# Kernel tuning notes

Measured on AMD Instinct MI355X. Metric: run time of the kernel, lower is better.

## Reference

```python
import jax, jax.numpy as jnp
import numpy as np
import math

WINDOW = 257
W = (WINDOW - 1) // 2      # 128
Q_CH = WINDOW + 1          # 258 (query chunk size / stride)
K_CH = WINDOW * 2          # 514 (key window size)


def compl_mod(m, n):
    return int(n * math.ceil(m / n) - m)


def setup_inputs() -> dict:
    key = jax.random.key(0)
    k1, k2, k3 = jax.random.split(key, 3)
    b, s, nh, h = 2, 4096, 16, 64
    q = jax.random.normal(k1, (b, s, nh, h), jnp.float32)
    k = jax.random.normal(k2, (b, s, nh, h), jnp.float32)
    v = jax.random.normal(k3, (b, s, nh, h), jnp.float32)
    return {"q": q, "k": k, "v": v}


def reference(q, k, v):
    b, s, nh, h = q.shape
    q = q * h ** (-0.5)
    q_pad = compl_mod(s, Q_CH)
    k_pad = compl_mod(s + 2 * W - K_CH, Q_CH)
    c = (s + q_pad) // Q_CH  # number of chunks

    # pad along sequence dim (q right-padded; k/v haloed by w on both sides)
    qp = jnp.pad(q, ((0, 0), (0, q_pad), (0, 0), (0, 0)))
    kp = jnp.pad(k, ((0, 0), (W, W + k_pad), (0, 0), (0, 0)))
    vp = jnp.pad(v, ((0, 0), (W, W + k_pad), (0, 0), (0, 0)))

    # unfold: q non-overlapping chunks, k/v overlapping windows (size K_CH, stride Q_CH)
    qw = qp.reshape(b, c, Q_CH, nh, h)                              # [b,c,q,nh,h]
    idx = (jnp.arange(c) * Q_CH)[:, None] + jnp.arange(K_CH)[None]  # [c,K_CH]
    kw = kp[:, idx]                                                 # [b,c,k,nh,h]
    vw = vp[:, idx]

    A = jnp.einsum('bcqnh,bcknh->bncqk', qw, kw)  # [b,nh,c,Q_CH,K_CH]

    # banded mask: valid iff i <= j <= i + 2w (True = masked)
    i = jnp.arange(Q_CH)[:, None]
    j = jnp.arange(K_CH)[None, :]
    base = ~((j >= i) & (j <= i + 2 * W))
    mask_left = base.at[:, :W].set(True)                    # first chunk: no left halo
    mask_right = base.at[:, K_CH - (W + k_pad):].set(True)  # last chunk: no right halo/pad
    if c > 1:
        mask = jnp.concatenate(
            [mask_left[None], jnp.broadcast_to(base, (c - 2, Q_CH, K_CH)), mask_right[None]], axis=0)
    else:
        mask = (mask_left | mask_right)[None]

    mask_value = -jnp.finfo(A.dtype).max
    A = jnp.where(mask[None, None], mask_value, A)
    A = jax.nn.softmax(A, axis=-1)  # dropout omitted (eval mode)

    z = jnp.einsum('bncqk,bcknh->bncqh', A, vw)       # [b,nh,c,Q_CH,h]
    z = z.reshape(b, nh, c * Q_CH, h)[:, :, :s]       # trim q padding
    return jnp.transpose(z, (0, 2, 1, 3))             # [b,s,nh,h]
```

## Files before the change

### kernel.cpp

```cpp
#include <hip/hip_runtime.h>

typedef _Float16 h16;
typedef __attribute__((ext_vector_type(2))) _Float16 f16x2;
typedef __attribute__((ext_vector_type(4))) _Float16 f16x4;
typedef __attribute__((ext_vector_type(2))) __fp16   fp16x2n;
typedef __attribute__((ext_vector_type(8))) _Float16 f16x8;
typedef __attribute__((ext_vector_type(4))) float f32x4;

#define S_LEN 4096
#define NHEAD 16
#define HDIM  64
#define WIN   128
#define TQ    128
#define NQT   (S_LEN / TQ)
#define NCHT  12
#define KSTR  72
#define VSTR2 40
#define SSTR  40
#define QSCALE 0.18033688011112042f

static __device__ __forceinline__ f16x2 pk(float a, float b) {
    fp16x2n r = __builtin_amdgcn_cvt_pkrtz(a, b);
    return __builtin_bit_cast(f16x2, r);
}

static __device__ __forceinline__ f16x8 cvt8(float4 a, float4 b) {
    f16x2 p0 = pk(a.x, a.y), p1 = pk(a.z, a.w);
    f16x2 p2 = pk(b.x, b.y), p3 = pk(b.z, b.w);
    f16x8 r;
    r[0]=p0[0]; r[1]=p0[1]; r[2]=p1[0]; r[3]=p1[1];
    r[4]=p2[0]; r[5]=p2[1]; r[6]=p3[0]; r[7]=p3[1];
    return r;
}

__global__ __launch_bounds__(512, 4)
void wattn(const float* __restrict__ Qg, const float* __restrict__ Kg,
           const float* __restrict__ Vg, float* __restrict__ Og)
{
    __shared__ h16 Kbuf[3][32 * KSTR];
    __shared__ h16 Vbuf[3][64 * VSTR2];
    __shared__ h16 Slds[8 * 16 * SSTR];

    const int tid  = threadIdx.x;
    const int wid  = tid >> 6;
    const int lane = tid & 63;
    const int l15  = lane & 15;
    const int quad = lane >> 4;

    int lin = blockIdx.x + NQT * (blockIdx.y + NHEAD * blockIdx.z);
    int nwg = NQT * NHEAD * gridDim.z;
    int swz = ((nwg & 7) == 0) ? ((lin & 7) * (nwg >> 3) + (lin >> 3)) : lin;
    const int bx   = swz & (NQT - 1);
    const int head = (swz / NQT) & (NHEAD - 1);
    const int b    = swz / (NQT * NHEAD);

    const int q0    = bx * TQ;
    const int kbase = q0 - WIN;
    const int rowstride = NHEAD * HDIM;

    const float* KB = Kg + ((long)b * S_LEN * NHEAD + head) * HDIM;
    const float* VB = Vg + ((long)b * S_LEN * NHEAD + head) * HDIM;

    const int srow = tid >> 4;
    const int ish  = tid & 15;
    const int sh0  = ish * 4;
    const int vkey = ((srow + (((ish >> 2) & 3) << 3)) & 31) ^ ((ish & 3) << 3);

    float4 kreg, vreg;
    #define SLOAD(i) do {                                                    \
        int kg_ = kbase + (i)*32 + srow;                                     \
        kg_ = kg_ < 0 ? 0 : (kg_ > S_LEN-1 ? S_LEN-1 : kg_);                 \
        const float* kp_ = KB + (long)kg_ * rowstride + sh0;                 \
        const float* vp_ = VB + (long)kg_ * rowstride + sh0;                 \
        kreg = *(const float4*)kp_;                                          \
        vreg = *(const float4*)vp_;                                          \
    } while (0)
    #define SWRITE(i) do {                                                   \
        int bi_ = (i) % 3;                                                   \
        f16x2 ka_ = pk(kreg.x, kreg.y), kb_ = pk(kreg.z, kreg.w);            \
        f16x4 kv_; kv_[0]=ka_[0]; kv_[1]=ka_[1]; kv_[2]=kb_[0]; kv_[3]=kb_[1];\
        *(f16x4*)&Kbuf[bi_][srow * KSTR + sh0] = kv_;                        \
        Vbuf[bi_][(sh0+0) * VSTR2 + vkey] = (h16)vreg.x;                     \
        Vbuf[bi_][(sh0+1) * VSTR2 + vkey] = (h16)vreg.y;                     \
        Vbuf[bi_][(sh0+2) * VSTR2 + vkey] = (h16)vreg.z;                     \
        Vbuf[bi_][(sh0+3) * VSTR2 + vkey] = (h16)vreg.w;                     \
    } while (0)

    SLOAD(0);

    f16x8 aQ0, aQ1;
    {
        const int qrow = q0 + wid * 16 + l15;
        const float* qp = Qg + ((long)(b * S_LEN + qrow) * NHEAD + head) * HDIM;
        float4 x0 = *(const float4*)(qp + quad*8);
        float4 x1 = *(const float4*)(qp + quad*8 + 4);
        float4 x2 = *(const float4*)(qp + 32 + quad*8);
        float4 x3 = *(const float4*)(qp + 32 + quad*8 + 4);
        x0.x*=QSCALE; x0.y*=QSCALE; x0.z*=QSCALE; x0.w*=QSCALE;
        x1.x*=QSCALE; x1.y*=QSCALE; x1.z*=QSCALE; x1.w*=QSCALE;
        x2.x*=QSCALE; x2.y*=QSCALE; x2.z*=QSCALE; x2.w*=QSCALE;
        x3.x*=QSCALE; x3.y*=QSCALE; x3.z*=QSCALE; x3.w*=QSCALE;
        aQ0 = cvt8(x0, x1);
        aQ1 = cvt8(x2, x3);
    }

    SWRITE(0);
    __syncthreads();

    int lo[4], hi[4];
    #pragma unroll
    for (int r = 0; r < 4; ++r) {
        int qg = q0 + wid*16 + quad*4 + r;
        lo[r] = (qg - WIN < 0) ? 0 : qg - WIN;
        hi[r] = (qg + WIN > S_LEN-1) ? S_LEN-1 : qg + WIN;
    }

    float l_r[4] = {0.f, 0.f, 0.f, 0.f};
    f32x4 Oacc[4];
    #pragma unroll
    for (int t = 0; t < 4; ++t) Oacc[t] = (f32x4){0.f,0.f,0.f,0.f};

    const int c0 = wid >> 1;
    h16* Sw = &Slds[wid * 16 * SSTR];
    const int pxw = quad << 3;
    const int pxr = (l15 & 12) << 1;

    for (int i = 0; i < NCHT; ++i) {
        if (i + 1 < NCHT) SLOAD(i + 1);

        if ((unsigned)(i - c0) < 9u) {
            const h16* Kb = Kbuf[i % 3];
            const h16* Vb = Vbuf[i % 3];

            f16x8 bK00 = *(const f16x8*)&Kb[ l15      * KSTR + quad*8];
            f16x8 bK01 = *(const f16x8*)&Kb[ l15      * KSTR + 32 + quad*8];
            f16x8 bK10 = *(const f16x8*)&Kb[(16+l15)  * KSTR + quad*8];
            f16x8 bK11 = *(const f16x8*)&Kb[(16+l15)  * KSTR + 32 + quad*8];

            f32x4 s0 = (f32x4){0.f,0.f,0.f,0.f};
            s0 = __builtin_amdgcn_mfma_f32_16x16x32_f16(aQ0, bK00, s0, 0, 0, 0);
            s0 = __builtin_amdgcn_mfma_f32_16x16x32_f16(aQ1, bK01, s0, 0, 0, 0);
            f32x4 s1 = (f32x4){0.f,0.f,0.f,0.f};
            s1 = __builtin_amdgcn_mfma_f32_16x16x32_f16(aQ0, bK10, s1, 0, 0, 0);
            s1 = __builtin_amdgcn_mfma_f32_16x16x32_f16(aQ1, bK11, s1, 0, 0, 0);

            const int col0 = kbase + i*32 + l15;
            const int col1 = col0 + 16;
            #pragma unroll
            for (int r = 0; r < 4; ++r) {
                float v0 = (col0 >= lo[r] && col0 <= hi[r]) ? s0[r] : -1e30f;
                float v1 = (col1 >= lo[r] && col1 <= hi[r]) ? s1[r] : -1e30f;
                float p0 = exp2f(v0);
                float p1 = exp2f(v1);
                l_r[r] += p0 + p1;
                Sw[(quad*4 + r) * SSTR + ( l15       ^ pxw)] = (h16)p0;
                Sw[(quad*4 + r) * SSTR + ((16 + l15) ^ pxw)] = (h16)p1;
            }

            __builtin_amdgcn_wave_barrier();

            f16x8 aP = *(const f16x8*)&Sw[l15 * SSTR + ((quad*8) ^ pxr)];
            #pragma unroll
            for (int t = 0; t < 4; ++t) {
                f16x8 bV = *(const f16x8*)&Vb[(t*16 + l15) * VSTR2 +
                                              (((quad*8 + (t << 3)) & 31) ^ pxr)];
                Oacc[t] = __builtin_amdgcn_mfma_f32_16x16x32_f16(aP, bV, Oacc[t], 0, 0, 0);
            }
            __builtin_amdgcn_wave_barrier();
        }

        if (i + 1 < NCHT) SWRITE(i + 1);
        __syncthreads();
    }
    #undef SLOAD
    #undef SWRITE

    float* op = Og + ((long)(b * S_LEN + q0 + wid*16) * NHEAD + head) * HDIM;
    #pragma unroll
    for (int r = 0; r < 4; ++r) {
        float l = l_r[r];
        l += __shfl_xor(l, 1);
        l += __shfl_xor(l, 2);
        l += __shfl_xor(l, 4);
        l += __shfl_xor(l, 8);
        float inv = 1.0f / l;
        #pragma unroll
        for (int t = 0; t < 4; ++t) {
            op[(quad*4 + r) * rowstride + t*16 + l15] = Oacc[t][r] * inv;
        }
    }
}

extern "C" void kernel_launch(void* const* d_in, const int* in_sizes, int n_in,
                              void* d_out, int out_size, void* d_ws, size_t ws_size,
                              hipStream_t stream) {
    const float* q = (const float*)d_in[0];
    const float* k = (const float*)d_in[1];
    const float* v = (const float*)d_in[2];
    float* out = (float*)d_out;
    const int batch = in_sizes[0] / (S_LEN * NHEAD * HDIM);
    dim3 grid(NQT, NHEAD, batch);
    wattn<<<grid, 512, 0, stream>>>(q, k, v, out);
}
```

Baseline: 149.6 us.

## Keep P in registers via transposed QK MFMA and cross-lane swizzles; deepen K/V prefetch

The QK^T MFMA operands are swapped, so each lane holds scores for one query row across four keys. The P tile is then repacked to fp16 and rearranged with ds_swizzle and shuffles directly into the A-operand layout for the PV MFMA. This removes the per-wave LDS staging buffer and its wave barriers. K/V global loads are now issued two chunks ahead, with the LDS write moved to the top of the loop. Row-sum reduction becomes a cheap two-step xor shuffle plus a broadcast at the end. In exchange there is more cross-lane permute work and higher register pressure from the deeper prefetch.

```diff
diff --git a/kernel.cpp b/kernel.cpp
--- a/kernel.cpp
+++ b/kernel.cpp
@@ -6,6 +6,7 @@
 typedef __attribute__((ext_vector_type(2))) __fp16   fp16x2n;
 typedef __attribute__((ext_vector_type(8))) _Float16 f16x8;
 typedef __attribute__((ext_vector_type(4))) float f32x4;
+typedef __attribute__((ext_vector_type(4))) int   i32x4;
 
 #define S_LEN 4096
 #define NHEAD 16
@@ -16,7 +17,6 @@
 #define NCHT  12
 #define KSTR  72
 #define VSTR2 40
-#define SSTR  40
 #define QSCALE 0.18033688011112042f
 
 static __device__ __forceinline__ f16x2 pk(float a, float b) {
@@ -39,7 +39,6 @@
 {
     __shared__ h16 Kbuf[3][32 * KSTR];
     __shared__ h16 Vbuf[3][64 * VSTR2];
-    __shared__ h16 Slds[8 * 16 * SSTR];
 
     const int tid  = threadIdx.x;
     const int wid  = tid >> 6;
@@ -105,28 +104,26 @@
     }
 
     SWRITE(0);
+    SLOAD(1);
     __syncthreads();
 
-    int lo[4], hi[4];
-    #pragma unroll
-    for (int r = 0; r < 4; ++r) {
-        int qg = q0 + wid*16 + quad*4 + r;
-        lo[r] = (qg - WIN < 0) ? 0 : qg - WIN;
-        hi[r] = (qg + WIN > S_LEN-1) ? S_LEN-1 : qg + WIN;
-    }
-
-    float l_r[4] = {0.f, 0.f, 0.f, 0.f};
+    const int qg = q0 + wid*16 + l15;
+    const int lo = (qg - WIN < 0) ? 0 : qg - WIN;
+    const int hi = (qg + WIN > S_LEN-1) ? S_LEN-1 : qg + WIN;
+    const unsigned span = (unsigned)(hi - lo);
+
+    float l_lane = 0.f;
     f32x4 Oacc[4];
     #pragma unroll
     for (int t = 0; t < 4; ++t) Oacc[t] = (f32x4){0.f,0.f,0.f,0.f};
 
     const int c0 = wid >> 1;
-    h16* Sw = &Slds[wid * 16 * SSTR];
-    const int pxw = quad << 3;
     const int pxr = (l15 & 12) << 1;
+    const int xl = (quad == 1 || quad == 2) ? (lane ^ 48) : lane;
 
     for (int i = 0; i < NCHT; ++i) {
-        if (i + 1 < NCHT) SLOAD(i + 1);
+        if (i + 1 < NCHT) SWRITE(i + 1);
+        if (i + 2 < NCHT) SLOAD(i + 2);
 
         if ((unsigned)(i - c0) < 9u) {
             const h16* Kb = Kbuf[i % 3];
@@ -138,55 +135,67 @@
             f16x8 bK11 = *(const f16x8*)&Kb[(16+l15)  * KSTR + 32 + quad*8];
 
             f32x4 s0 = (f32x4){0.f,0.f,0.f,0.f};
-            s0 = __builtin_amdgcn_mfma_f32_16x16x32_f16(aQ0, bK00, s0, 0, 0, 0);
-            s0 = __builtin_amdgcn_mfma_f32_16x16x32_f16(aQ1, bK01, s0, 0, 0, 0);
+            s0 = __builtin_amdgcn_mfma_f32_16x16x32_f16(bK00, aQ0, s0, 0, 0, 0);
+            s0 = __builtin_amdgcn_mfma_f32_16x16x32_f16(bK01, aQ1, s0, 0, 0, 0);
             f32x4 s1 = (f32x4){0.f,0.f,0.f,0.f};
-            s1 = __builtin_amdgcn_mfma_f32_16x16x32_f16(aQ0, bK10, s1, 0, 0, 0);
-            s1 = __builtin_amdgcn_mfma_f32_16x16x32_f16(aQ1, bK11, s1, 0, 0, 0);
-
-            const int col0 = kbase + i*32 + l15;
-            const int col1 = col0 + 16;
+            s1 = __builtin_amdgcn_mfma_f32_16x16x32_f16(bK10, aQ0, s1, 0, 0, 0);
+            s1 = __builtin_amdgcn_mfma_f32_16x16x32_f16(bK11, aQ1, s1, 0, 0, 0);
+
+            const int colb = kbase + i*32 + quad*4;
+            float pl[4], ph[4];
             #pragma unroll
             for (int r = 0; r < 4; ++r) {
-                float v0 = (col0 >= lo[r] && col0 <= hi[r]) ? s0[r] : -1e30f;
-                float v1 = (col1 >= lo[r] && col1 <= hi[r]) ? s1[r] : -1e30f;
-                float p0 = exp2f(v0);
-                float p1 = exp2f(v1);
-                l_r[r] += p0 + p1;
-                Sw[(quad*4 + r) * SSTR + ( l15       ^ pxw)] = (h16)p0;
-                Sw[(quad*4 + r) * SSTR + ((16 + l15) ^ pxw)] = (h16)p1;
+                int c_ = colb + r;
+                float v0 = ((unsigned)(c_      - lo) <= span) ? s0[r] : -1e30f;
+                float v1 = ((unsigned)(c_ + 16 - lo) <= span) ? s1[r] : -1e30f;
+                pl[r] = exp2f(v0);
+                ph[r] = exp2f(v1);
             }
-
-            __builtin_amdgcn_wave_barrier();
-
-            f16x8 aP = *(const f16x8*)&Sw[l15 * SSTR + ((quad*8) ^ pxr)];
+            l_lane += ((pl[0]+pl[1]) + (pl[2]+pl[3]))
+                    + ((ph[0]+ph[1]) + (ph[2]+ph[3]));
+
+            int u0 = __builtin_bit_cast(int, pk(pl[0], pl[1]));
+            int u1 = __builtin_bit_cast(int, pk(pl[2], pl[3]));
+            int u2 = __builtin_bit_cast(int, pk(ph[0], ph[1]));
+            int u3 = __builtin_bit_cast(int, pk(ph[2], ph[3]));
+            {
+                const bool q0b = (quad & 1);
+                int s0w = q0b ? u0 : u2;
+                int s1w = q0b ? u1 : u3;
+                int r0 = __builtin_amdgcn_ds_swizzle(s0w, 0x401F);
+                int r1 = __builtin_amdgcn_ds_swizzle(s1w, 0x401F);
+                if (q0b) { u0 = r0; u1 = r1; } else { u2 = r0; u3 = r1; }
+            }
+            u0 = __shfl(u0, xl);  u1 = __shfl(u1, xl);
+            u2 = __shfl(u2, xl);  u3 = __shfl(u3, xl);
+            i32x4 uu; uu[0]=u0; uu[1]=u1; uu[2]=u2; uu[3]=u3;
+            f16x8 aP = __builtin_bit_cast(f16x8, uu);
+
             #pragma unroll
             for (int t = 0; t < 4; ++t) {
                 f16x8 bV = *(const f16x8*)&Vb[(t*16 + l15) * VSTR2 +
                                               (((quad*8 + (t << 3)) & 31) ^ pxr)];
                 Oacc[t] = __builtin_amdgcn_mfma_f32_16x16x32_f16(aP, bV, Oacc[t], 0, 0, 0);
             }
-            __builtin_amdgcn_wave_barrier();
         }
 
-        if (i + 1 < NCHT) SWRITE(i + 1);
         __syncthreads();
     }
     #undef SLOAD
     #undef SWRITE
 
+    float l = l_lane;
+    l += __shfl_xor(l, 16);
+    l += __shfl_xor(l, 32);
+    const float inv = 1.0f / l;
+
     float* op = Og + ((long)(b * S_LEN + q0 + wid*16) * NHEAD + head) * HDIM;
     #pragma unroll
     for (int r = 0; r < 4; ++r) {
-        float l = l_r[r];
-        l += __shfl_xor(l, 1);
-        l += __shfl_xor(l, 2);
-        l += __shfl_xor(l, 4);
-        l += __shfl_xor(l, 8);
-        float inv = 1.0f / l;
+        float invr = __shfl(inv, quad*4 + r);
         #pragma unroll
         for (int t = 0; t < 4; ++t) {
-            op[(quad*4 + r) * rowstride + t*16 + l15] = Oacc[t][r] * inv;
+            op[(quad*4 + r) * rowstride + t*16 + l15] = Oacc[t][r] * invr;
         }
     }
 }
```

New measurement: 148.3 us. About the same (-0.9%).
